# Performance work log

Measured on AMD Instinct MI355X. Metric: run time of the kernel, lower is better.

The kernel has to match this reference:

```python
import jax, jax.numpy as jnp
import numpy as np
import math

B, S, D, H, WIN = 2, 4096, 512, 8, 50
DK = D // H


def setup_inputs() -> dict:
    key = jax.random.key(0)
    ks = jax.random.split(key, 10)
    scale = 0.02
    return {
        "x": jax.random.normal(ks[0], (B, S, D), dtype=jnp.float32),
        "opcode_types": jax.random.randint(ks[1], (B, S), 0, 10, dtype=jnp.int64),
        "Wq": jax.random.normal(ks[2], (D, D), dtype=jnp.float32) * scale,
        "bq": jnp.zeros((D,), dtype=jnp.float32),
        "Wk": jax.random.normal(ks[3], (D, D), dtype=jnp.float32) * scale,
        "bk": jnp.zeros((D,), dtype=jnp.float32),
        "Wv": jax.random.normal(ks[4], (D, D), dtype=jnp.float32) * scale,
        "bv": jnp.zeros((D,), dtype=jnp.float32),
        "Wo": jax.random.normal(ks[5], (D, D), dtype=jnp.float32) * scale,
        "bo": jnp.zeros((D,), dtype=jnp.float32),
    }


def reference(x, opcode_types, Wq, bq, Wk, bk, Wv, bv, Wo, bo):
    b, s, d = x.shape
    # Linear projections (torch Linear: x @ W.T + b), split heads -> [B,H,S,DK]
    q = (x @ Wq.T + bq).reshape(b, s, H, DK).transpose(0, 2, 1, 3)
    k = (x @ Wk.T + bk).reshape(b, s, H, DK).transpose(0, 2, 1, 3)
    v = (x @ Wv.T + bv).reshape(b, s, H, DK).transpose(0, 2, 1, 3)

    pos = jnp.arange(s)
    window = jnp.abs(pos[:, None] - pos[None, :]) <= WIN          # [S,S]
    ctrl_cols = (opcode_types == 0).any(axis=0)                   # [S]
    allow = window | ctrl_cols[None, :]                           # [S,S]

    scores = jnp.einsum("bhqd,bhkd->bhqk", q, k) / math.sqrt(DK)  # [B,H,S,S]
    scores = jnp.where(allow[None, None], scores, jnp.float32(-1e9))
    attn = jax.nn.softmax(scores, axis=-1)
    attn = jnp.nan_to_num(attn, nan=0.0)
    out = jnp.einsum("bhqk,bhkd->bhqd", attn, v)                  # [B,H,S,DK]
    out = out.transpose(0, 2, 1, 3).reshape(b, s, d)
    return out @ Wo.T + bo
```

## Files before the change

kernel.cpp:

```cpp
#include <hip/hip_runtime.h>
#include <hip/hip_bf16.h>
#include <math.h>

#define B_ 2
#define S_ 4096
#define D_ 512
#define H_ 8
#define DK_ 64
#define WIN_ 50
#define NGT 32
#define QSCALE 0.18033688011112042f

typedef __attribute__((ext_vector_type(8))) short short8;
typedef __attribute__((ext_vector_type(4))) float f32x4;
typedef __attribute__((ext_vector_type(4))) unsigned short us4;
typedef unsigned short ushort_t;

__device__ __forceinline__ unsigned short f2bf(float f) {
    unsigned u = __builtin_bit_cast(unsigned, f);
    u += 0x7FFF + ((u >> 16) & 1);
    return (unsigned short)(u >> 16);
}
__device__ __forceinline__ float bf2f(unsigned short h) {
    return __builtin_bit_cast(float, ((unsigned)h) << 16);
}
__device__ __forceinline__ unsigned cvt_pk_bf16(float lo, float hi) {
    unsigned r;
    asm("v_cvt_pk_bf16_f32 %0, %1, %2" : "=v"(r) : "v"(lo), "v"(hi));
    return r;
}
__device__ __forceinline__ float v_exp2(float x) {
    float r;
    asm("v_exp_f32 %0, %1\n\ts_nop 0" : "=v"(r) : "v"(x));
    return r;
}

__global__ __launch_bounds__(256) void prep_all(const float* __restrict__ x,
                                                const float* __restrict__ W0,
                                                const float* __restrict__ W1,
                                                const float* __restrict__ W2,
                                                const float* __restrict__ W3,
                                                const int* __restrict__ opcode,
                                                ushort_t* __restrict__ xh,
                                                ushort_t* __restrict__ whb,
                                                ushort_t* __restrict__ wol,
                                                int* __restrict__ glist,
                                                int* __restrict__ gcount) {
    const int bid = blockIdx.x;
    const int t = threadIdx.x;
    if (bid < 4096) {
        int i = bid * 256 + t;
        f32x4 v = ((const f32x4*)x)[i];
        us4 hv;
        for (int e = 0; e < 4; ++e) hv[e] = f2bf(v[e]);
        ((us4*)xh)[i] = hv;
    } else if (bid < 5120) {
        int b2 = bid - 4096;
        int wz = b2 >> 8, inner = b2 & 255;
        const float* src = (wz == 0) ? W0 : (wz == 1) ? W1 : (wz == 2) ? W2 : W3;
        int i = inner * 256 + t;
        f32x4 v = ((const f32x4*)src)[i];
        us4 hv, lv;
        for (int e = 0; e < 4; ++e) {
            unsigned short hb = f2bf(v[e]);
            hv[e] = hb;
            lv[e] = f2bf(v[e] - bf2f(hb));
        }
        ((us4*)(whb + (size_t)wz * D_ * D_))[i] = hv;
        if (wz == 3) ((us4*)wol)[i] = lv;
    } else {
        __shared__ int cnts[256];
        unsigned fl = 0; int c = 0;
        for (int k = 0; k < 16; ++k) {
            int col = t * 16 + k;
            int flag = (opcode[col] == 0) | (opcode[S_ + col] == 0);
            fl |= (unsigned)flag << k; c += flag;
        }
        cnts[t] = c;
        __syncthreads();
        for (int off = 1; off < 256; off <<= 1) {
            int v = cnts[t];
            int a = (t >= off) ? cnts[t - off] : 0;
            __syncthreads();
            cnts[t] = v + a;
            __syncthreads();
        }
        int base = cnts[t] - c;
        for (int k = 0; k < 16; ++k)
            if ((fl >> k) & 1) glist[base++] = t * 16 + k;
        int G = cnts[255];
        if (t == 255) gcount[0] = G;
        for (int k = 0; k < 8; ++k) {
            int idx = G + t + k * 256;
            if (idx < S_) glist[idx] = -1;
        }
    }
}

__device__ __forceinline__ void gemm_core1(const ushort_t* __restrict__ A,
                                           const ushort_t* __restrict__ Bw,
                                           ushort_t (&LDS)[2][8192],
                                           int m0, int n0, int t,
                                           f32x4 (&acc)[4][4]) {
    const int lane = t & 63, wave = t >> 6;
    const int lrow = lane & 15, lkg = lane >> 4;
    const int wr = wave >> 1, wc = wave & 1;
    const ushort_t* srcs[2] = {A, Bw};
    const int row0[2] = {m0, n0};

    auto stage = [&](int buf, int k0) {
        #pragma unroll
        for (int it = 0; it < 4; ++it) {
            int c = it * 4 + wave;
            int tile = c >> 3;
            int kg = (c >> 1) & 3;
            int r = ((c & 1) << 6) | lane;
            const ushort_t* g = srcs[tile] + (size_t)(row0[tile] + r) * 512 + k0 + kg * 8;
            __builtin_amdgcn_global_load_lds(
                (const __attribute__((address_space(1))) void*)g,
                (__attribute__((address_space(3))) void*)(&LDS[buf][c * 512]),
                16, 0, 0);
        }
    };

    stage(0, 0);
    __syncthreads();

    const int aoff = lkg * 1024 + (wr * 64 + lrow) * 8;
    const int boff = 4096 + lkg * 1024 + (wc * 64 + lrow) * 8;
    int cur = 0;
    for (int ks = 0; ks < 16; ++ks) {
        if (ks < 15) stage(cur ^ 1, (ks + 1) * 32);
        const ushort_t* Lb = LDS[cur];
        short8 ah[4], bh[4];
        #pragma unroll
        for (int m = 0; m < 4; ++m) ah[m] = *(const short8*)(Lb + aoff + m * 128);
        #pragma unroll
        for (int n = 0; n < 4; ++n) bh[n] = *(const short8*)(Lb + boff + n * 128);
        #pragma unroll
        for (int m = 0; m < 4; ++m)
            #pragma unroll
            for (int n = 0; n < 4; ++n)
                acc[m][n] = __builtin_amdgcn_mfma_f32_16x16x32_bf16(ah[m], bh[n], acc[m][n], 0, 0, 0);
        __syncthreads();
        cur ^= 1;
    }
}

__device__ __forceinline__ void gemm_core3(const ushort_t* __restrict__ Ah,
                                           const ushort_t* __restrict__ Al,
                                           const ushort_t* __restrict__ Bh,
                                           const ushort_t* __restrict__ Bl,
                                           ushort_t (&LDS)[2][16384],
                                           int m0, int n0, int t,
                                           f32x4 (&acc)[4][4]) {
    const int lane = t & 63, wave = t >> 6;
    const int lrow = lane & 15, lkg = lane >> 4;
    const int wr = wave >> 1, wc = wave & 1;
    const ushort_t* srcs[4] = {Ah, Al, Bh, Bl};
    const int row0[4] = {m0, m0, n0, n0};

    auto stage = [&](int buf, int k0) {
        #pragma unroll
        for (int it = 0; it < 8; ++it) {
            int c = it * 4 + wave;
            int tile = c >> 3;
            int kg = (c >> 1) & 3;
            int r = ((c & 1) << 6) | lane;
            const ushort_t* g = srcs[tile] + (size_t)(row0[tile] + r) * 512 + k0 + kg * 8;
            __builtin_amdgcn_global_load_lds(
                (const __attribute__((address_space(1))) void*)g,
                (__attribute__((address_space(3))) void*)(&LDS[buf][c * 512]),
                16, 0, 0);
        }
    };

    stage(0, 0);
    __syncthreads();

    const int aoff = lkg * 1024 + (wr * 64 + lrow) * 8;
    const int boff = 2 * 4096 + lkg * 1024 + (wc * 64 + lrow) * 8;
    int cur = 0;
    for (int ks = 0; ks < 16; ++ks) {
        if (ks < 15) stage(cur ^ 1, (ks + 1) * 32);
        const ushort_t* Lb = LDS[cur];
        short8 ah[4], al[4], bh[4], bl[4];
        #pragma unroll
        for (int m = 0; m < 4; ++m) {
            ah[m] = *(const short8*)(Lb + aoff + m * 128);
            al[m] = *(const short8*)(Lb + 4096 + aoff + m * 128);
        }
        #pragma unroll
        for (int n = 0; n < 4; ++n) {
            bh[n] = *(const short8*)(Lb + boff + n * 128);
            bl[n] = *(const short8*)(Lb + 4096 + boff + n * 128);
        }
        #pragma unroll
        for (int m = 0; m < 4; ++m)
            #pragma unroll
            for (int n = 0; n < 4; ++n) {
                acc[m][n] = __builtin_amdgcn_mfma_f32_16x16x32_bf16(ah[m], bh[n], acc[m][n], 0, 0, 0);
                acc[m][n] = __builtin_amdgcn_mfma_f32_16x16x32_bf16(al[m], bh[n], acc[m][n], 0, 0, 0);
                acc[m][n] = __builtin_amdgcn_mfma_f32_16x16x32_bf16(ah[m], bl[n], acc[m][n], 0, 0, 0);
            }
        __syncthreads();
        cur ^= 1;
    }
}

__global__ __launch_bounds__(256) void gemm_qkv(const ushort_t* __restrict__ xh,
                                                const ushort_t* __restrict__ whb,
                                                const float* __restrict__ bq,
                                                const float* __restrict__ bk,
                                                const float* __restrict__ bv,
                                                ushort_t* __restrict__ qb,
                                                char* __restrict__ bandimg) {
    __shared__ ushort_t LDS[2][8192];
    const int z = blockIdx.z;
    const int t = threadIdx.x;
    const ushort_t* Wz = whb + (size_t)z * D_ * D_;
    const int lane = t & 63, wave = t >> 6;
    const int lrow = lane & 15, lkg = lane >> 4;
    const int wr = wave >> 1, wc = wave & 1;

    f32x4 acc[4][4];
    for (int m = 0; m < 4; ++m)
        for (int n = 0; n < 4; ++n)
            acc[m][n] = f32x4{0.f, 0.f, 0.f, 0.f};

    if (z == 2) {
        const int m0 = blockIdx.y * 128, n0 = blockIdx.x * 128;
        gemm_core1(xh, Wz, LDS, m0, n0, t, acc);
        for (int m = 0; m < 4; ++m) {
            int s_base = m0 + wr * 64 + m * 16 + lkg * 4;
            int bb = s_base >> 12, s0 = s_base & (S_ - 1);
            int jt = s0 >> 6, jr0 = s0 & 63;
            for (int n = 0; n < 4; ++n) {
                int col = n0 + wc * 64 + n * 16 + lrow;
                float bs = bv[col];
                int hh = col >> 6, dk = col & 63;
                us4 pk;
                for (int r = 0; r < 4; ++r) pk[r] = f2bf(acc[m][n][r] + bs);
                char* img = bandimg + (((size_t)(bb * H_ + hh)) * 64 + jt) * 16384 + 8192;
                *(us4*)(img + ((dk * 128 + jr0 * 2) ^ ((dk & 7) << 4))) = pk;
            }
        }
    } else {
        const int m0 = blockIdx.x * 128, n0 = blockIdx.y * 128;
        gemm_core1(Wz, xh, LDS, m0, n0, t, acc);
        const float* bias = (z == 0) ? bq : bk;
        for (int m = 0; m < 4; ++m) {
            int d_base = m0 + wr * 64 + m * 16 + lkg * 4;
            f32x4 b4 = *(const f32x4*)(bias + d_base);
            int hh = d_base >> 6, dkb = d_base & 63;
            for (int n = 0; n < 4; ++n) {
                int s = n0 + wc * 64 + n * 16 + lrow;
                int bb = s >> 12, sl = s & (S_ - 1);
                us4 pk;
                if (z == 0) {
                    for (int r = 0; r < 4; ++r) pk[r] = f2bf((acc[m][n][r] + b4[r]) * QSCALE);
                    *(us4*)(qb + (((size_t)(bb * H_ + hh) * S_) + sl) * DK_ + dkb) = pk;
                } else {
                    for (int r = 0; r < 4; ++r) pk[r] = f2bf(acc[m][n][r] + b4[r]);
                    int jt = sl >> 6, jr = sl & 63;
                    char* img = bandimg + (((size_t)(bb * H_ + hh)) * 64 + jt) * 16384;
                    *(us4*)(img + ((jr * 128 + dkb * 2) ^ ((jr & 7) << 4))) = pk;
                }
            }
        }
    }
}

__global__ __launch_bounds__(256) void gemm_fin(const ushort_t* __restrict__ Woh,
                                                const ushort_t* __restrict__ Wol,
                                                const ushort_t* __restrict__ aoh,
                                                const ushort_t* __restrict__ aol,
                                                const float* __restrict__ bias,
                                                float* __restrict__ outp) {
    __shared__ ushort_t LDS[2][16384];
    const int t = threadIdx.x;
    const int lane = t & 63, wave = t >> 6;
    const int lrow = lane & 15, lkg = lane >> 4;
    const int wr = wave >> 1, wc = wave & 1;
    const int m0 = blockIdx.x * 128, n0 = blockIdx.y * 128;

    f32x4 acc[4][4];
    for (int m = 0; m < 4; ++m)
        for (int n = 0; n < 4; ++n)
            acc[m][n] = f32x4{0.f, 0.f, 0.f, 0.f};
    gemm_core3(Woh, Wol, aoh, aol, LDS, m0, n0, t, acc);

    for (int m = 0; m < 4; ++m) {
        int d_base = m0 + wr * 64 + m * 16 + lkg * 4;
        f32x4 b4 = *(const f32x4*)(bias + d_base);
        for (int n = 0; n < 4; ++n) {
            int s = n0 + wc * 64 + n * 16 + lrow;
            f32x4 o;
            for (int r = 0; r < 4; ++r) o[r] = acc[m][n][r] + b4[r];
            *(f32x4*)(outp + (size_t)s * D_ + d_base) = o;
        }
    }
}

__global__ __launch_bounds__(256) void prep_glob(const char* __restrict__ bandimg,
                                                 char* __restrict__ globimg,
                                                 const int* __restrict__ glist,
                                                 const int* __restrict__ gcount) {
    int G = gcount[0];
    int gc = blockIdx.x;
    if (gc * 64 >= G) return;
    int h = blockIdx.y, b = blockIdx.z;
    int t = threadIdx.x;
    __shared__ int jl[64];
    if (t < 64) { int gi = gc * 64 + t; jl[t] = (gi < G) ? glist[gi] : -1; }
    __syncthreads();
    const size_t bh = (size_t)(b * H_ + h);
    char* dst = globimg + (bh * NGT + gc) * 16384;
    {
        int c = t >> 2, q = t & 3;
        int jj = jl[c];
        #pragma unroll
        for (int p = 0; p < 2; ++p) {
            int o_dst = c * 128 + q * 32 + p * 16;
            short8 val;
            if (jj >= 0) {
                int jr = jj & 63, jt = jj >> 6;
                const char* src = bandimg + (bh * 64 + jt) * 16384;
                val = *(const short8*)(src + ((jr * 128 + q * 32 + p * 16) ^ ((jr & 7) << 4)));
            } else {
                for (int e = 0; e < 8; ++e) val[e] = 0;
            }
            *(short8*)(dst + (o_dst ^ ((c & 7) << 4))) = val;
        }
    }
    {
        int d = t >> 2, qq = t & 3;
        short8 v0, v1;
        #pragma unroll 16
        for (int i = 0; i < 16; ++i) {
            int c = qq * 16 + i;
            int jj = jl[c];
            ushort_t val = 0;
            if (jj >= 0) {
                int jr = jj & 63, jt = jj >> 6;
                const char* src = bandimg + (bh * 64 + jt) * 16384 + 8192;
                val = *(const ushort_t*)(src + ((d * 128 + jr * 2) ^ ((d & 7) << 4)));
            }
            if (i < 8) v0[i] = val; else v1[i - 8] = val;
        }
        int o = d * 128 + qq * 32;
        *(short8*)(dst + 8192 + (o ^ ((d & 7) << 4))) = v0;
        *(short8*)(dst + 8192 + ((o + 16) ^ ((d & 7) << 4))) = v1;
    }
}

__global__ __launch_bounds__(512) void attn_mfma5(const ushort_t* __restrict__ Qp,
                                                  const char* __restrict__ bandimg,
                                                  const char* __restrict__ globimg,
                                                  const int* __restrict__ glist,
                                                  const int* __restrict__ gcount,
                                                  ushort_t* __restrict__ AOh,
                                                  ushort_t* __restrict__ AOl) {
    __shared__ char buf[2][16384];
    __shared__ ushort_t Ps[8 * 16 * 64];

    const int t = threadIdx.x, lane = t & 63, wave = t >> 6;
    const int q = lane & 15, g = lane >> 4;
    const int bid = blockIdx.x;
    const int bh_lin = bid & 15;
    const int b = bh_lin >> 3, h = bh_lin & 7;
    const int i0 = (bid >> 4) * 128;
    const size_t headoff = ((size_t)(b * H_ + h)) * S_ * DK_;
    const int iq = i0 + wave * 16 + q;
    const int iqm = iq - WIN_;

    short8 qa[2];
    {
        const ushort_t* qrow = Qp + headoff + (size_t)iq * DK_;
        qa[0] = *(const short8*)(qrow + 8 * g);
        qa[1] = *(const short8*)(qrow + 32 + 8 * g);
    }

    f32x4 Oa[4];
    for (int n = 0; n < 4; ++n) Oa[n] = f32x4{0.f, 0.f, 0.f, 0.f};
    float m_st = -1e30f, l_st = 0.f;

    int jlo = i0 - WIN_;
    int jt_lo = (jlo < 0) ? 0 : (jlo >> 6);
    int jhi = i0 + 127 + WIN_; if (jhi > S_ - 1) jhi = S_ - 1;
    int jt_hi = jhi >> 6;
    int nband = jt_hi - jt_lo + 1;
    const int G = gcount[0];
    int nglob = (G + 63) >> 6; if (nglob > NGT) nglob = NGT;
    int nchunk = nband + nglob;

    const size_t bh = (size_t)(b * H_ + h);

    unsigned needmask = 0;
    {
        int wmin = i0 - WIN_, wmax = i0 + 127 + WIN_;
        for (int gc = 0; gc < nglob; ++gc) {
            int lo = glist[gc * 64];
            int hidx = (gc * 64 + 63 < G) ? (gc * 64 + 63) : (G - 1);
            int hi = glist[hidx];
            bool nm = (lo <= wmax && hi >= wmin) || (gc == nglob - 1 && (G & 63));
            needmask |= (unsigned)nm << gc;
        }
    }

    int koff[4][2], poffw[4], poffr[2];
    #pragma unroll
    for (int n = 0; n < 4; ++n) {
        int row = n * 16 + q;
        #pragma unroll
        for (int kt = 0; kt < 2; ++kt)
            koff[n][kt] = (row * 128 + g * 16 + kt * 64) ^ ((row & 7) << 4);
        poffw[n] = (q * 128 + n * 32 + g * 8) ^ ((q & 7) << 4);
    }
    #pragma unroll
    for (int kt = 0; kt < 2; ++kt)
        poffr[kt] = (q * 128 + g * 16 + kt * 64) ^ ((q & 7) << 4);

    const char* band_base = bandimg + (bh * 64 + jt_lo) * 16384;
    const char* glob_base = globimg + (bh * NGT) * 16384;

    auto stage = [&](int ch, int nb) {
        const char* img = (ch < nband) ? (band_base + (size_t)ch * 16384)
                                       : (glob_base + (size_t)(ch - nband) * 16384);
        #pragma unroll
        for (int i = 0; i < 2; ++i) {
            int seg = wave * 2 + i;
            __builtin_amdgcn_global_load_lds(
                (const __attribute__((address_space(1))) void*)(img + seg * 1024 + lane * 16),
                (__attribute__((address_space(3))) void*)(buf[nb] + seg * 1024),
                16, 0, 0);
        }
    };

    stage(0, 0);
    __syncthreads();

    int cur = 0;
    for (int ch = 0; ch < nchunk; ++ch) {
        if (ch + 1 < nchunk) stage(ch + 1, cur ^ 1);
        const bool isband = ch < nband;
        const int cbase = isband ? (jt_lo + ch) * 64 : 0;
        const int gbase = (ch - nband) * 64;
        const char* Kb = buf[cur];
        const char* Vb = buf[cur] + 8192;

        f32x4 sc[4];
        for (int n = 0; n < 4; ++n) sc[n] = f32x4{0.f, 0.f, 0.f, 0.f};
        #pragma unroll
        for (int n = 0; n < 4; ++n)
            #pragma unroll
            for (int kt = 0; kt < 2; ++kt) {
                short8 ka = *(const short8*)(Kb + koff[n][kt]);
                sc[n] = __builtin_amdgcn_mfma_f32_16x16x32_bf16(ka, qa[kt], sc[n], 0, 0, 0);
            }

        float pm;
        bool nm = isband || ((needmask >> (ch - nband)) & 1);
        if (nm) {
            pm = -1e30f;
            if (isband) {
                #pragma unroll
                for (int n = 0; n < 4; ++n) {
                    int jb = cbase + n * 16 + 4 * g;
                    #pragma unroll
                    for (int r = 0; r < 4; ++r) {
                        bool inwin = (unsigned)(jb + r - iqm) <= 2 * WIN_;
                        float s = inwin ? sc[n][r] : -1e30f;
                        sc[n][r] = s;
                        pm = fmaxf(pm, s);
                    }
                }
            } else {
                #pragma unroll
                for (int n = 0; n < 4; ++n) {
                    int4 J = *(const int4*)(glist + gbase + n * 16 + g * 4);
                    int js[4] = {J.x, J.y, J.z, J.w};
                    #pragma unroll
                    for (int r = 0; r < 4; ++r) {
                        int jj = js[r];
                        bool inwin = (unsigned)(jj - iqm) <= 2 * WIN_;
                        bool allow = (jj >= 0) && !inwin;
                        float s = allow ? sc[n][r] : -1e30f;
                        sc[n][r] = s;
                        pm = fmaxf(pm, s);
                    }
                }
            }
        } else {
            float a0 = fmaxf(fmaxf(sc[0][0], sc[0][1]), fmaxf(sc[0][2], sc[0][3]));
            float a1 = fmaxf(fmaxf(sc[1][0], sc[1][1]), fmaxf(sc[1][2], sc[1][3]));
            float a2 = fmaxf(fmaxf(sc[2][0], sc[2][1]), fmaxf(sc[2][2], sc[2][3]));
            float a3 = fmaxf(fmaxf(sc[3][0], sc[3][1]), fmaxf(sc[3][2], sc[3][3]));
            pm = fmaxf(fmaxf(a0, a1), fmaxf(a2, a3));
        }
        pm = fmaxf(pm, __shfl_xor(pm, 16, 64));
        pm = fmaxf(pm, __shfl_xor(pm, 32, 64));

        bool skip = __all(pm <= m_st);
        float fac = 1.0f;
        if (!skip) {
            float mn = fmaxf(m_st, pm);
            fac = v_exp2(m_st - mn);
            m_st = mn;
        }
        float rs = 0.f;
        #pragma unroll
        for (int n = 0; n < 4; ++n)
            #pragma unroll
            for (int r = 0; r < 4; ++r) {
                float p = v_exp2(sc[n][r] - m_st);
                sc[n][r] = p;
                rs += p;
            }
        rs += __shfl_xor(rs, 16, 64);
        rs += __shfl_xor(rs, 32, 64);
        l_st = skip ? (l_st + rs) : (l_st * fac + rs);

        ushort_t* Pw = Ps + wave * 1024;
        #pragma unroll
        for (int n = 0; n < 4; ++n) {
            unsigned pk0 = cvt_pk_bf16(sc[n][0], sc[n][1]);
            unsigned pk1 = cvt_pk_bf16(sc[n][2], sc[n][3]);
            *(unsigned long long*)((char*)Pw + poffw[n]) =
                ((unsigned long long)pk1 << 32) | pk0;
        }

        if (!skip) {
            #pragma unroll
            for (int n = 0; n < 4; ++n)
                #pragma unroll
                for (int r = 0; r < 4; ++r) Oa[n][r] *= fac;
        }

        short8 pa[2];
        #pragma unroll
        for (int kt = 0; kt < 2; ++kt)
            pa[kt] = *(const short8*)((char*)Pw + poffr[kt]);
        #pragma unroll
        for (int n = 0; n < 4; ++n)
            #pragma unroll
            for (int kt = 0; kt < 2; ++kt) {
                short8 va = *(const short8*)(Vb + koff[n][kt]);
                Oa[n] = __builtin_amdgcn_mfma_f32_16x16x32_bf16(va, pa[kt], Oa[n], 0, 0, 0);
            }
        __syncthreads();
        cur ^= 1;
    }

    float inv = 1.0f / l_st;
    #pragma unroll
    for (int n = 0; n < 4; ++n) {
        us4 ph, pl;
        #pragma unroll
        for (int r = 0; r < 4; ++r) {
            float v = Oa[n][r] * inv;
            unsigned short hb = f2bf(v);
            ph[r] = hb;
            pl[r] = f2bf(v - bf2f(hb));
        }
        size_t base = ((size_t)b * S_ + iq) * D_ + h * DK_ + (n * 16 + g * 4);
        *(us4*)(AOh + base) = ph;
        *(us4*)(AOl + base) = pl;
    }
}

extern "C" void kernel_launch(void* const* d_in, const int* in_sizes, int n_in,
                              void* d_out, int out_size, void* d_ws, size_t ws_size,
                              hipStream_t stream) {
    const float* x      = (const float*)d_in[0];
    const int*   opcode = (const int*)d_in[1];
    const float* Wq = (const float*)d_in[2];
    const float* bq = (const float*)d_in[3];
    const float* Wk = (const float*)d_in[4];
    const float* bk = (const float*)d_in[5];
    const float* Wv = (const float*)d_in[6];
    const float* bv = (const float*)d_in[7];
    const float* Wo = (const float*)d_in[8];
    const float* bo = (const float*)d_in[9];
    float* out = (float*)d_out;

    char* ws = (char*)d_ws;
    const size_t bsd = (size_t)B_ * S_ * D_;
    const size_t bf_bytes = bsd * sizeof(ushort_t);
    const size_t w_bytes  = (size_t)D_ * D_ * sizeof(ushort_t);

    ushort_t* qb  = (ushort_t*)(ws);
    ushort_t* xh  = (ushort_t*)(ws + bf_bytes);
    ushort_t* aol = (ushort_t*)(ws + 2 * bf_bytes);
    ushort_t* aoh = xh;
    char* wbase = ws + 3 * bf_bytes;
    ushort_t* whb = (ushort_t*)wbase;
    ushort_t* wol = (ushort_t*)(wbase + 4 * w_bytes);
    char* bandimg = wbase + 5 * w_bytes;
    char* globimg = bandimg + (size_t)16 * 64 * 16384;
    int* glist  = (int*)(globimg + (size_t)16 * NGT * 16384);
    int* gcount = glist + S_;

    prep_all<<<5121, 256, 0, stream>>>(x, Wq, Wk, Wv, Wo, opcode,
                                       xh, whb, wol, glist, gcount);

    gemm_qkv<<<dim3(D_ / 128, (B_ * S_) / 128, 3), 256, 0, stream>>>(
        xh, whb, bq, bk, bv, qb, bandimg);

    prep_glob<<<dim3(NGT, H_, B_), 256, 0, stream>>>(bandimg, globimg, glist, gcount);

    attn_mfma5<<<dim3(512), 512, 0, stream>>>(
        qb, bandimg, globimg, glist, gcount, aoh, aol);

    gemm_fin<<<dim3(D_ / 128, (B_ * S_) / 128), 256, 0, stream>>>(
        whb + 3 * (size_t)D_ * D_, wol, aoh, aol, bo, out);
}
```

Measured before the change: 196.0 us.

## Switch pipeline from bf16 to fp16 and drop split-precision output projection

All intermediate operands (x, weights, Q/K/V, probabilities, attention output) now use fp16 instead of bf16, with f16 MFMA instructions throughout. Because fp16 has more mantissa bits, the hi/lo split of Wo and the attention output is removed, so the final GEMM drops from three MFMAs per step to one and no longer reads the lo buffers. The final GEMM is retiled to 64-row blocks to keep enough workgroups, and s_setprio is placed around the attention MFMA sections. fp16's narrower range risks overflow in the projections or probabilities, and accuracy now rests on the fp16 mantissa.

```diff
diff --git a/kernel.cpp b/kernel.cpp
--- a/kernel.cpp
+++ b/kernel.cpp
@@ -11,22 +11,18 @@
 #define NGT 32
 #define QSCALE 0.18033688011112042f
 
-typedef __attribute__((ext_vector_type(8))) short short8;
+typedef __attribute__((ext_vector_type(8))) _Float16 half8;
 typedef __attribute__((ext_vector_type(4))) float f32x4;
 typedef __attribute__((ext_vector_type(4))) unsigned short us4;
 typedef unsigned short ushort_t;
 
-__device__ __forceinline__ unsigned short f2bf(float f) {
-    unsigned u = __builtin_bit_cast(unsigned, f);
-    u += 0x7FFF + ((u >> 16) & 1);
-    return (unsigned short)(u >> 16);
-}
-__device__ __forceinline__ float bf2f(unsigned short h) {
-    return __builtin_bit_cast(float, ((unsigned)h) << 16);
-}
-__device__ __forceinline__ unsigned cvt_pk_bf16(float lo, float hi) {
+__device__ __forceinline__ unsigned short f2h(float f) {
+    _Float16 h = (_Float16)f;
+    return __builtin_bit_cast(unsigned short, h);
+}
+__device__ __forceinline__ unsigned cvt_pk_f16(float lo, float hi) {
     unsigned r;
-    asm("v_cvt_pk_bf16_f32 %0, %1, %2" : "=v"(r) : "v"(lo), "v"(hi));
+    asm("v_cvt_pkrtz_f16_f32 %0, %1, %2" : "=v"(r) : "v"(lo), "v"(hi));
     return r;
 }
 __device__ __forceinline__ float v_exp2(float x) {
@@ -43,7 +39,6 @@
                                                 const int* __restrict__ opcode,
                                                 ushort_t* __restrict__ xh,
                                                 ushort_t* __restrict__ whb,
-                                                ushort_t* __restrict__ wol,
                                                 int* __restrict__ glist,
                                                 int* __restrict__ gcount) {
     const int bid = blockIdx.x;
@@ -52,7 +47,7 @@
         int i = bid * 256 + t;
         f32x4 v = ((const f32x4*)x)[i];
         us4 hv;
-        for (int e = 0; e < 4; ++e) hv[e] = f2bf(v[e]);
+        for (int e = 0; e < 4; ++e) hv[e] = f2h(v[e]);
         ((us4*)xh)[i] = hv;
     } else if (bid < 5120) {
         int b2 = bid - 4096;
@@ -60,14 +55,9 @@
         const float* src = (wz == 0) ? W0 : (wz == 1) ? W1 : (wz == 2) ? W2 : W3;
         int i = inner * 256 + t;
         f32x4 v = ((const f32x4*)src)[i];
-        us4 hv, lv;
-        for (int e = 0; e < 4; ++e) {
-            unsigned short hb = f2bf(v[e]);
-            hv[e] = hb;
-            lv[e] = f2bf(v[e] - bf2f(hb));
-        }
+        us4 hv;
+        for (int e = 0; e < 4; ++e) hv[e] = f2h(v[e]);
         ((us4*)(whb + (size_t)wz * D_ * D_))[i] = hv;
-        if (wz == 3) ((us4*)wol)[i] = lv;
     } else {
         __shared__ int cnts[256];
         unsigned fl = 0; int c = 0;
@@ -132,77 +122,16 @@
     for (int ks = 0; ks < 16; ++ks) {
         if (ks < 15) stage(cur ^ 1, (ks + 1) * 32);
         const ushort_t* Lb = LDS[cur];
-        short8 ah[4], bh[4];
-        #pragma unroll
-        for (int m = 0; m < 4; ++m) ah[m] = *(const short8*)(Lb + aoff + m * 128);
-        #pragma unroll
-        for (int n = 0; n < 4; ++n) bh[n] = *(const short8*)(Lb + boff + n * 128);
+        half8 ah[4], bh[4];
+        #pragma unroll
+        for (int m = 0; m < 4; ++m) ah[m] = *(const half8*)(Lb + aoff + m * 128);
+        #pragma unroll
+        for (int n = 0; n < 4; ++n) bh[n] = *(const half8*)(Lb + boff + n * 128);
         #pragma unroll
         for (int m = 0; m < 4; ++m)
             #pragma unroll
             for (int n = 0; n < 4; ++n)
-                acc[m][n] = __builtin_amdgcn_mfma_f32_16x16x32_bf16(ah[m], bh[n], acc[m][n], 0, 0, 0);
-        __syncthreads();
-        cur ^= 1;
-    }
-}
-
-__device__ __forceinline__ void gemm_core3(const ushort_t* __restrict__ Ah,
-                                           const ushort_t* __restrict__ Al,
-                                           const ushort_t* __restrict__ Bh,
-                                           const ushort_t* __restrict__ Bl,
-                                           ushort_t (&LDS)[2][16384],
-                                           int m0, int n0, int t,
-                                           f32x4 (&acc)[4][4]) {
-    const int lane = t & 63, wave = t >> 6;
-    const int lrow = lane & 15, lkg = lane >> 4;
-    const int wr = wave >> 1, wc = wave & 1;
-    const ushort_t* srcs[4] = {Ah, Al, Bh, Bl};
-    const int row0[4] = {m0, m0, n0, n0};
-
-    auto stage = [&](int buf, int k0) {
-        #pragma unroll
-        for (int it = 0; it < 8; ++it) {
-            int c = it * 4 + wave;
-            int tile = c >> 3;
-            int kg = (c >> 1) & 3;
-            int r = ((c & 1) << 6) | lane;
-            const ushort_t* g = srcs[tile] + (size_t)(row0[tile] + r) * 512 + k0 + kg * 8;
-            __builtin_amdgcn_global_load_lds(
-                (const __attribute__((address_space(1))) void*)g,
-                (__attribute__((address_space(3))) void*)(&LDS[buf][c * 512]),
-                16, 0, 0);
-        }
-    };
-
-    stage(0, 0);
-    __syncthreads();
-
-    const int aoff = lkg * 1024 + (wr * 64 + lrow) * 8;
-    const int boff = 2 * 4096 + lkg * 1024 + (wc * 64 + lrow) * 8;
-    int cur = 0;
-    for (int ks = 0; ks < 16; ++ks) {
-        if (ks < 15) stage(cur ^ 1, (ks + 1) * 32);
-        const ushort_t* Lb = LDS[cur];
-        short8 ah[4], al[4], bh[4], bl[4];
-        #pragma unroll
-        for (int m = 0; m < 4; ++m) {
-            ah[m] = *(const short8*)(Lb + aoff + m * 128);
-            al[m] = *(const short8*)(Lb + 4096 + aoff + m * 128);
-        }
-        #pragma unroll
-        for (int n = 0; n < 4; ++n) {
-            bh[n] = *(const short8*)(Lb + boff + n * 128);
-            bl[n] = *(const short8*)(Lb + 4096 + boff + n * 128);
-        }
-        #pragma unroll
-        for (int m = 0; m < 4; ++m)
-            #pragma unroll
-            for (int n = 0; n < 4; ++n) {
-                acc[m][n] = __builtin_amdgcn_mfma_f32_16x16x32_bf16(ah[m], bh[n], acc[m][n], 0, 0, 0);
-                acc[m][n] = __builtin_amdgcn_mfma_f32_16x16x32_bf16(al[m], bh[n], acc[m][n], 0, 0, 0);
-                acc[m][n] = __builtin_amdgcn_mfma_f32_16x16x32_bf16(ah[m], bl[n], acc[m][n], 0, 0, 0);
-            }
+                acc[m][n] = __builtin_amdgcn_mfma_f32_16x16x32_f16(ah[m], bh[n], acc[m][n], 0, 0, 0);
         __syncthreads();
         cur ^= 1;
     }
@@ -240,7 +169,7 @@
                 float bs = bv[col];
                 int hh = col >> 6, dk = col & 63;
                 us4 pk;
-                for (int r = 0; r < 4; ++r) pk[r] = f2bf(acc[m][n][r] + bs);
+                for (int r = 0; r < 4; ++r) pk[r] = f2h(acc[m][n][r] + bs);
                 char* img = bandimg + (((size_t)(bb * H_ + hh)) * 64 + jt) * 16384 + 8192;
                 *(us4*)(img + ((dk * 128 + jr0 * 2) ^ ((dk & 7) << 4))) = pk;
             }
@@ -258,10 +187,10 @@
                 int bb = s >> 12, sl = s & (S_ - 1);
                 us4 pk;
                 if (z == 0) {
-                    for (int r = 0; r < 4; ++r) pk[r] = f2bf((acc[m][n][r] + b4[r]) * QSCALE);
+                    for (int r = 0; r < 4; ++r) pk[r] = f2h((acc[m][n][r] + b4[r]) * QSCALE);
                     *(us4*)(qb + (((size_t)(bb * H_ + hh) * S_) + sl) * DK_ + dkb) = pk;
                 } else {
-                    for (int r = 0; r < 4; ++r) pk[r] = f2bf(acc[m][n][r] + b4[r]);
+                    for (int r = 0; r < 4; ++r) pk[r] = f2h(acc[m][n][r] + b4[r]);
                     int jt = sl >> 6, jr = sl & 63;
                     char* img = bandimg + (((size_t)(bb * H_ + hh)) * 64 + jt) * 16384;
                     *(us4*)(img + ((jr * 128 + dkb * 2) ^ ((jr & 7) << 4))) = pk;
@@ -272,26 +201,65 @@
 }
 
 __global__ __launch_bounds__(256) void gemm_fin(const ushort_t* __restrict__ Woh,
-                                                const ushort_t* __restrict__ Wol,
                                                 const ushort_t* __restrict__ aoh,
-                                                const ushort_t* __restrict__ aol,
                                                 const float* __restrict__ bias,
                                                 float* __restrict__ outp) {
-    __shared__ ushort_t LDS[2][16384];
+    __shared__ ushort_t LDS[2][6144];
     const int t = threadIdx.x;
     const int lane = t & 63, wave = t >> 6;
     const int lrow = lane & 15, lkg = lane >> 4;
     const int wr = wave >> 1, wc = wave & 1;
-    const int m0 = blockIdx.x * 128, n0 = blockIdx.y * 128;
-
-    f32x4 acc[4][4];
-    for (int m = 0; m < 4; ++m)
+    const int m0 = blockIdx.x * 64, n0 = blockIdx.y * 128;
+
+    auto stage = [&](int buf, int k0) {
+        #pragma unroll
+        for (int it = 0; it < 3; ++it) {
+            int c = it * 4 + wave;
+            const ushort_t* g;
+            if (c < 4) {
+                g = Woh + (size_t)(m0 + lane) * 512 + k0 + c * 8;
+            } else {
+                int s2 = c - 4;
+                int kg = s2 >> 1, rh = s2 & 1;
+                g = aoh + (size_t)(n0 + rh * 64 + lane) * 512 + k0 + kg * 8;
+            }
+            __builtin_amdgcn_global_load_lds(
+                (const __attribute__((address_space(1))) void*)g,
+                (__attribute__((address_space(3))) void*)(&LDS[buf][c * 512]),
+                16, 0, 0);
+        }
+    };
+
+    f32x4 acc[2][4];
+    for (int m = 0; m < 2; ++m)
         for (int n = 0; n < 4; ++n)
             acc[m][n] = f32x4{0.f, 0.f, 0.f, 0.f};
-    gemm_core3(Woh, Wol, aoh, aol, LDS, m0, n0, t, acc);
-
-    for (int m = 0; m < 4; ++m) {
-        int d_base = m0 + wr * 64 + m * 16 + lkg * 4;
+
+    stage(0, 0);
+    __syncthreads();
+
+    const int aoff = lkg * 512 + (wr * 32 + lrow) * 8;
+    const int boff = 2048 + lkg * 1024 + (wc * 64 + lrow) * 8;
+    int cur = 0;
+    for (int ks = 0; ks < 16; ++ks) {
+        if (ks < 15) stage(cur ^ 1, (ks + 1) * 32);
+        const ushort_t* Lb = LDS[cur];
+        half8 ah[2], bh[4];
+        #pragma unroll
+        for (int m = 0; m < 2; ++m) ah[m] = *(const half8*)(Lb + aoff + m * 128);
+        #pragma unroll
+        for (int n = 0; n < 4; ++n) bh[n] = *(const half8*)(Lb + boff + n * 128);
+        #pragma unroll
+        for (int m = 0; m < 2; ++m)
+            #pragma unroll
+            for (int n = 0; n < 4; ++n)
+                acc[m][n] = __builtin_amdgcn_mfma_f32_16x16x32_f16(ah[m], bh[n], acc[m][n], 0, 0, 0);
+        __syncthreads();
+        cur ^= 1;
+    }
+
+    for (int m = 0; m < 2; ++m) {
+        int d_base = m0 + wr * 32 + m * 16 + lkg * 4;
         f32x4 b4 = *(const f32x4*)(bias + d_base);
         for (int n = 0; n < 4; ++n) {
             int s = n0 + wc * 64 + n * 16 + lrow;
@@ -322,20 +290,21 @@
         #pragma unroll
         for (int p = 0; p < 2; ++p) {
             int o_dst = c * 128 + q * 32 + p * 16;
-            short8 val;
+            __attribute__((ext_vector_type(8))) short val;
             if (jj >= 0) {
                 int jr = jj & 63, jt = jj >> 6;
                 const char* src = bandimg + (bh * 64 + jt) * 16384;
-                val = *(const short8*)(src + ((jr * 128 + q * 32 + p * 16) ^ ((jr & 7) << 4)));
+                val = *(const __attribute__((ext_vector_type(8))) short*)
+                      (src + ((jr * 128 + q * 32 + p * 16) ^ ((jr & 7) << 4)));
             } else {
                 for (int e = 0; e < 8; ++e) val[e] = 0;
             }
-            *(short8*)(dst + (o_dst ^ ((c & 7) << 4))) = val;
+            *(__attribute__((ext_vector_type(8))) short*)(dst + (o_dst ^ ((c & 7) << 4))) = val;
         }
     }
     {
         int d = t >> 2, qq = t & 3;
-        short8 v0, v1;
+        __attribute__((ext_vector_type(8))) short v0, v1;
         #pragma unroll 16
         for (int i = 0; i < 16; ++i) {
             int c = qq * 16 + i;
@@ -349,18 +318,17 @@
             if (i < 8) v0[i] = val; else v1[i - 8] = val;
         }
         int o = d * 128 + qq * 32;
-        *(short8*)(dst + 8192 + (o ^ ((d & 7) << 4))) = v0;
-        *(short8*)(dst + 8192 + ((o + 16) ^ ((d & 7) << 4))) = v1;
-    }
-}
-
-__global__ __launch_bounds__(512) void attn_mfma5(const ushort_t* __restrict__ Qp,
+        *(__attribute__((ext_vector_type(8))) short*)(dst + 8192 + (o ^ ((d & 7) << 4))) = v0;
+        *(__attribute__((ext_vector_type(8))) short*)(dst + 8192 + ((o + 16) ^ ((d & 7) << 4))) = v1;
+    }
+}
+
+__global__ __launch_bounds__(512) void attn_mfma6(const ushort_t* __restrict__ Qp,
                                                   const char* __restrict__ bandimg,
                                                   const char* __restrict__ globimg,
                                                   const int* __restrict__ glist,
                                                   const int* __restrict__ gcount,
-                                                  ushort_t* __restrict__ AOh,
-                                                  ushort_t* __restrict__ AOl) {
+                                                  ushort_t* __restrict__ AO) {
     __shared__ char buf[2][16384];
     __shared__ ushort_t Ps[8 * 16 * 64];
 
@@ -374,11 +342,11 @@
     const int iq = i0 + wave * 16 + q;
     const int iqm = iq - WIN_;
 
-    short8 qa[2];
+    half8 qa[2];
     {
         const ushort_t* qrow = Qp + headoff + (size_t)iq * DK_;
-        qa[0] = *(const short8*)(qrow + 8 * g);
-        qa[1] = *(const short8*)(qrow + 32 + 8 * g);
+        qa[0] = *(const half8*)(qrow + 8 * g);
+        qa[1] = *(const half8*)(qrow + 32 + 8 * g);
     }
 
     f32x4 Oa[4];
@@ -451,13 +419,15 @@
 
         f32x4 sc[4];
         for (int n = 0; n < 4; ++n) sc[n] = f32x4{0.f, 0.f, 0.f, 0.f};
+        __builtin_amdgcn_s_setprio(1);
         #pragma unroll
         for (int n = 0; n < 4; ++n)
             #pragma unroll
             for (int kt = 0; kt < 2; ++kt) {
-                short8 ka = *(const short8*)(Kb + koff[n][kt]);
-                sc[n] = __builtin_amdgcn_mfma_f32_16x16x32_bf16(ka, qa[kt], sc[n], 0, 0, 0);
-            }
+                half8 ka = *(const half8*)(Kb + koff[n][kt]);
+                sc[n] = __builtin_amdgcn_mfma_f32_16x16x32_f16(ka, qa[kt], sc[n], 0, 0, 0);
+            }
+        __builtin_amdgcn_s_setprio(0);
 
         float pm;
         bool nm = isband || ((needmask >> (ch - nband)) & 1);
@@ -524,8 +494,8 @@
         ushort_t* Pw = Ps + wave * 1024;
         #pragma unroll
         for (int n = 0; n < 4; ++n) {
-            unsigned pk0 = cvt_pk_bf16(sc[n][0], sc[n][1]);
-            unsigned pk1 = cvt_pk_bf16(sc[n][2], sc[n][3]);
+            unsigned pk0 = cvt_pk_f16(sc[n][0], sc[n][1]);
+            unsigned pk1 = cvt_pk_f16(sc[n][2], sc[n][3]);
             *(unsigned long long*)((char*)Pw + poffw[n]) =
                 ((unsigned long long)pk1 << 32) | pk0;
         }
@@ -537,17 +507,19 @@
                 for (int r = 0; r < 4; ++r) Oa[n][r] *= fac;
         }
 
-        short8 pa[2];
+        half8 pa[2];
         #pragma unroll
         for (int kt = 0; kt < 2; ++kt)
-            pa[kt] = *(const short8*)((char*)Pw + poffr[kt]);
+            pa[kt] = *(const half8*)((char*)Pw + poffr[kt]);
+        __builtin_amdgcn_s_setprio(1);
         #pragma unroll
         for (int n = 0; n < 4; ++n)
             #pragma unroll
             for (int kt = 0; kt < 2; ++kt) {
-                short8 va = *(const short8*)(Vb + koff[n][kt]);
-                Oa[n] = __builtin_amdgcn_mfma_f32_16x16x32_bf16(va, pa[kt], Oa[n], 0, 0, 0);
-            }
+                half8 va = *(const half8*)(Vb + koff[n][kt]);
+                Oa[n] = __builtin_amdgcn_mfma_f32_16x16x32_f16(va, pa[kt], Oa[n], 0, 0, 0);
+            }
+        __builtin_amdgcn_s_setprio(0);
         __syncthreads();
         cur ^= 1;
     }
@@ -555,17 +527,11 @@
     float inv = 1.0f / l_st;
     #pragma unroll
     for (int n = 0; n < 4; ++n) {
-        us4 ph, pl;
-        #pragma unroll
-        for (int r = 0; r < 4; ++r) {
-            float v = Oa[n][r] * inv;
-            unsigned short hb = f2bf(v);
-            ph[r] = hb;
-            pl[r] = f2bf(v - bf2f(hb));
-        }
+        us4 ph;
+        #pragma unroll
+        for (int r = 0; r < 4; ++r) ph[r] = f2h(Oa[n][r] * inv);
         size_t base = ((size_t)b * S_ + iq) * D_ + h * DK_ + (n * 16 + g * 4);
-        *(us4*)(AOh + base) = ph;
-        *(us4*)(AOl + base) = pl;
+        *(us4*)(AO + base) = ph;
     }
 }
 
@@ -586,32 +552,30 @@
 
     char* ws = (char*)d_ws;
     const size_t bsd = (size_t)B_ * S_ * D_;
-    const size_t bf_bytes = bsd * sizeof(ushort_t);
+    const size_t hf_bytes = bsd * sizeof(ushort_t);
     const size_t w_bytes  = (size_t)D_ * D_ * sizeof(ushort_t);
 
-    ushort_t* qb  = (ushort_t*)(ws);
-    ushort_t* xh  = (ushort_t*)(ws + bf_bytes);
-    ushort_t* aol = (ushort_t*)(ws + 2 * bf_bytes);
-    ushort_t* aoh = xh;
-    char* wbase = ws + 3 * bf_bytes;
+    ushort_t* qb = (ushort_t*)(ws);
+    ushort_t* xh = (ushort_t*)(ws + hf_bytes);
+    ushort_t* ao = xh;
+    char* wbase = ws + 2 * hf_bytes;
     ushort_t* whb = (ushort_t*)wbase;
-    ushort_t* wol = (ushort_t*)(wbase + 4 * w_bytes);
-    char* bandimg = wbase + 5 * w_bytes;
+    char* bandimg = wbase + 4 * w_bytes;
     char* globimg = bandimg + (size_t)16 * 64 * 16384;
     int* glist  = (int*)(globimg + (size_t)16 * NGT * 16384);
     int* gcount = glist + S_;
 
     prep_all<<<5121, 256, 0, stream>>>(x, Wq, Wk, Wv, Wo, opcode,
-                                       xh, whb, wol, glist, gcount);
+                                       xh, whb, glist, gcount);
 
     gemm_qkv<<<dim3(D_ / 128, (B_ * S_) / 128, 3), 256, 0, stream>>>(
         xh, whb, bq, bk, bv, qb, bandimg);
 
     prep_glob<<<dim3(NGT, H_, B_), 256, 0, stream>>>(bandimg, globimg, glist, gcount);
 
-    attn_mfma5<<<dim3(512), 512, 0, stream>>>(
-        qb, bandimg, globimg, glist, gcount, aoh, aol);
-
-    gemm_fin<<<dim3(D_ / 128, (B_ * S_) / 128), 256, 0, stream>>>(
-        whb + 3 * (size_t)D_ * D_, wol, aoh, aol, bo, out);
-}
+    attn_mfma6<<<dim3(512), 512, 0, stream>>>(
+        qb, bandimg, globimg, glist, gcount, ao);
+
+    gemm_fin<<<dim3(D_ / 64, (B_ * S_) / 128), 256, 0, stream>>>(
+        whb + 3 * (size_t)D_ * D_, ao, bo, out);
+}
```

New measurement: 188.6 us. 3.8% less time.
